# Performance work log

Hardware: AMD Instinct MI355X
Metric: run time of the kernel (lower is better)

## Reference

```python
import jax, jax.numpy as jnp
import numpy as np

N_NODES = 50000
N_GRAPHS = 1024


def _linear_params(key, fan_in, fan_out):
    k1, k2 = jax.random.split(key)
    lim = 1.0 / np.sqrt(fan_in)
    W = jax.random.uniform(k1, (fan_in, fan_out), minval=-lim, maxval=lim, dtype=jnp.float32)
    b = jax.random.uniform(k2, (fan_out,), minval=-lim, maxval=lim, dtype=jnp.float32)
    return W, b


def gcn_conv(x, W, b, src, dst, n):
    # PyG GCNConv: D^{-1/2} (A + I) D^{-1/2} X W + b, deg counted at target after self-loops
    h = x @ W                                   # [N, out]
    deg = jnp.zeros((n,), h.dtype).at[dst].add(1.0) + 1.0
    dinv = jax.lax.rsqrt(deg)
    norm = dinv[src] * dinv[dst]                # [E]
    msg = h[src] * norm[:, None]                # [E, out] (dominant traffic)
    agg = jax.ops.segment_sum(msg, dst, num_segments=n)
    agg = agg + h * (dinv * dinv)[:, None]      # self-loop contribution
    return agg + b


def setup_inputs() -> dict:
    key = jax.random.key(0)
    ks = jax.random.split(key, 16)
    x = jax.random.normal(ks[0], (N_NODES, 64), dtype=jnp.float32)
    edge_index = jax.random.randint(ks[1], (2, 800000), 0, N_NODES, dtype=jnp.int64)
    batch = jnp.sort(jax.random.randint(ks[2], (N_NODES,), 0, N_GRAPHS, dtype=jnp.int64))
    fingerprint_features = jax.random.uniform(ks[3], (N_GRAPHS, 2048), dtype=jnp.float32)
    func_groups = jax.random.uniform(ks[4], (N_GRAPHS, 167), dtype=jnp.float32)
    W1, b1 = _linear_params(ks[5], 64, 128)
    W2, b2 = _linear_params(ks[6], 128, 256)
    W3, b3 = _linear_params(ks[7], 256, 256)
    Wr1, br1 = _linear_params(ks[8], 128, 256)
    Wr2, br2 = _linear_params(ks[9], 256, 256)
    Wfp, bfp = _linear_params(ks[10], 2048, 256)
    Wfg, bfg = _linear_params(ks[11], 167, 256)
    attn_W = jax.random.uniform(ks[12], (256, 256), dtype=jnp.float32)
    Wfc, bfc = _linear_params(ks[13], 256, 1)
    return dict(x=x, edge_index=edge_index, batch=batch,
                fingerprint_features=fingerprint_features, func_groups=func_groups,
                W1=W1, b1=b1, W2=W2, b2=b2, W3=W3, b3=b3,
                Wr1=Wr1, br1=br1, Wr2=Wr2, br2=br2,
                Wfp=Wfp, bfp=bfp, Wfg=Wfg, bfg=bfg,
                attn_W=attn_W, Wfc=Wfc, bfc=bfc)


def reference(x, edge_index, batch, fingerprint_features, func_groups,
              W1, b1, W2, b2, W3, b3, Wr1, br1, Wr2, br2,
              Wfp, bfp, Wfg, bfg, attn_W, Wfc, bfc):
    n = x.shape[0]
    src, dst = edge_index[0], edge_index[1]
    x1 = jax.nn.relu(gcn_conv(x, W1, b1, src, dst, n))            # [N,128]
    # dropout inactive (eval mode)
    x2 = jax.nn.relu(gcn_conv(x1, W2, b2, src, dst, n) + x1 @ Wr1 + br1)  # [N,256]
    x3 = jax.nn.relu(gcn_conv(x2, W3, b3, src, dst, n) + x2 @ Wr2 + br2)  # [N,256]
    fp = jax.nn.relu(fingerprint_features @ Wfp + bfp)            # [B,256]
    fg = jax.nn.relu(func_groups @ Wfg + bfg)                     # [B,256]
    attn = jax.nn.softmax(x3 @ attn_W, axis=1)                    # [N,256]
    xw = attn * x3
    sums = jax.ops.segment_sum(xw, batch, num_segments=N_GRAPHS)  # [B,256]
    cnt = jax.ops.segment_sum(jnp.ones((n,), xw.dtype), batch, num_segments=N_GRAPHS)
    pooled = sums / jnp.maximum(cnt, 1.0)[:, None]                # global_mean_pool
    out = (pooled + fp + fg) @ Wfc + bfc                          # [B,1]
    return out.reshape(-1, 1)
```

## Files before the change

### kernel.cpp

```cpp
#include <hip/hip_runtime.h>
#include <math.h>

#define CDIV(a,b) (((a)+(b)-1)/(b))

typedef __attribute__((ext_vector_type(8))) short bf16x8;
typedef __attribute__((ext_vector_type(4))) float f32x4;

__device__ inline unsigned short f2bf(float f) {
    unsigned int u = __float_as_uint(f);
    u += 0x7fffu + ((u >> 16) & 1u);
    return (unsigned short)(u >> 16);
}
__device__ inline float bf2f(unsigned short h) { return __uint_as_float(((unsigned int)h) << 16); }
__device__ inline unsigned short f2h(float f) {
    _Float16 h = (_Float16)f;
    return *(unsigned short*)&h;
}
__device__ inline float h2f(unsigned short u) {
    _Float16 h = *(_Float16*)&u;
    return (float)h;
}

__global__ void deg_count_kernel(const int* __restrict__ dst, int* __restrict__ deg, int E) {
    int e = blockIdx.x * blockDim.x + threadIdx.x;
    if (e < E) atomicAdd(&deg[dst[e]], 1);
}

__global__ void dinv_kernel(const int* __restrict__ deg, float* __restrict__ dinv, int N) {
    int i = blockIdx.x * blockDim.x + threadIdx.x;
    if (i < N) dinv[i] = rsqrtf((float)deg[i] + 1.0f);
}

__global__ void chunk_sum_kernel(const int* __restrict__ deg, int* __restrict__ csum, int N) {
    __shared__ int ws[4];
    int c = blockIdx.x, t = threadIdx.x;
    int base = c * 1024;
    int s = 0;
    for (int i = t; i < 1024; i += 256) { int idx = base + i; s += (idx < N) ? deg[idx] : 0; }
    for (int o = 32; o; o >>= 1) s += __shfl_xor(s, o);
    if ((t & 63) == 0) ws[t >> 6] = s;
    __syncthreads();
    if (t == 0) csum[c] = ws[0] + ws[1] + ws[2] + ws[3];
}

__global__ void chunk_scan_kernel(int* __restrict__ csum, int nc) {
    int t = threadIdx.x;
    int v = (t < nc) ? csum[t] : 0;
    int x = v;
    #pragma unroll
    for (int o = 1; o < 64; o <<= 1) { int y = __shfl_up(x, o, 64); if (t >= o) x += y; }
    if (t < nc) csum[t] = x - v;
}

__global__ void chunk_scan_apply_kernel(const int* __restrict__ deg, const int* __restrict__ cbase,
                                        int* __restrict__ off, int N, int E) {
    __shared__ int wsum[16];
    int c = blockIdx.x;
    int t = threadIdx.x;
    int lane = t & 63, wid = t >> 6;
    int i = c * 1024 + t;
    int v = (i < N) ? deg[i] : 0;
    int x = v;
    #pragma unroll
    for (int o = 1; o < 64; o <<= 1) { int y = __shfl_up(x, o, 64); if (lane >= o) x += y; }
    if (lane == 63) wsum[wid] = x;
    __syncthreads();
    if (wid == 0) {
        int wv = (lane < 16) ? wsum[lane] : 0;
        #pragma unroll
        for (int o = 1; o < 16; o <<= 1) { int y = __shfl_up(wv, o, 64); if (lane >= o) wv += y; }
        if (lane < 16) wsum[lane] = wv;
    }
    __syncthreads();
    int wexcl = wid ? wsum[wid - 1] : 0;
    if (i < N) off[i] = cbase[c] + wexcl + x - v;
    if (i == N) off[N] = E;
}

__global__ void csr_fill_kernel(const int* __restrict__ src, const int* __restrict__ dst,
                                const int* __restrict__ off, int* __restrict__ pos,
                                int* __restrict__ csr_src, int E) {
    int e = blockIdx.x * blockDim.x + threadIdx.x;
    if (e >= E) return;
    int s = src[e], d = dst[e];
    int p = off[d] + atomicAdd(&pos[d], 1);
    csr_src[p] = s;
}

__global__ void split_kernel(const float* __restrict__ src, unsigned short* __restrict__ hi,
                             unsigned short* __restrict__ lo, long long total) {
    long long idx = (long long)blockIdx.x * blockDim.x + threadIdx.x;
    if (idx >= total) return;
    float v = src[idx];
    unsigned short h = f2bf(v);
    hi[idx] = h;
    lo[idx] = f2bf(v - bf2f(h));
}

__global__ void f32_to_f16_kernel(const float* __restrict__ src, unsigned short* __restrict__ dst,
                                  long long total) {
    long long idx = (long long)blockIdx.x * blockDim.x + threadIdx.x;
    if (idx >= total) return;
    dst[idx] = f2h(src[idx]);
}

__global__ void wsplit_t_kernel(const float* __restrict__ src, int K, int N,
                                unsigned short* __restrict__ dsth, unsigned short* __restrict__ dstl,
                                int ldt, int koff) {
    int idx = blockIdx.x * blockDim.x + threadIdx.x;
    if (idx >= K * N) return;
    int col = idx / K;
    int k = idx - col * K;
    float v = src[(size_t)k * N + col];
    unsigned short h = f2bf(v);
    size_t o = (size_t)col * ldt + koff + k;
    dsth[o] = h;
    dstl[o] = f2bf(v - bf2f(h));
}

__global__ void bsum_kernel(const float* __restrict__ a, const float* __restrict__ b,
                            float* __restrict__ dst, int n) {
    int j = blockIdx.x * blockDim.x + threadIdx.x;
    if (j < n) dst[j] = a[j] + b[j];
}

template<int F>
__global__ __launch_bounds__(F) void gcn_gather_kernel(
        const unsigned short* __restrict__ h16, int ldh,
        const float* __restrict__ dinv, const int* __restrict__ off,
        const int* __restrict__ csr_src,
        unsigned short* __restrict__ outh, unsigned short* __restrict__ outl,
        int ldo, int cofo) {
    const int n = blockIdx.x;
    const int j = threadIdx.x;
    float dd = dinv[n];
    float acc = h2f(h16[(size_t)n * ldh + j]) * dd * dd;
    const int e1 = off[n + 1];
    int e = off[n];
    for (; e + 4 <= e1; e += 4) {
        int s0 = csr_src[e], s1 = csr_src[e + 1], s2 = csr_src[e + 2], s3 = csr_src[e + 3];
        float n0 = dinv[s0] * dd, n1 = dinv[s1] * dd, n2 = dinv[s2] * dd, n3 = dinv[s3] * dd;
        float h0 = h2f(h16[(size_t)s0 * ldh + j]);
        float h1 = h2f(h16[(size_t)s1 * ldh + j]);
        float h2 = h2f(h16[(size_t)s2 * ldh + j]);
        float h3 = h2f(h16[(size_t)s3 * ldh + j]);
        acc += h0 * n0; acc += h1 * n1; acc += h2 * n2; acc += h3 * n3;
    }
    for (; e < e1; ++e) {
        int s0 = csr_src[e];
        acc += h2f(h16[(size_t)s0 * ldh + j]) * (dinv[s0] * dd);
    }
    size_t o = (size_t)n * ldo + cofo + j;
    unsigned short hv = f2bf(acc);
    outh[o] = hv;
    outl[o] = f2bf(acc - bf2f(hv));
}

__global__ __launch_bounds__(256) void mfma_gemm_kernel(
        const unsigned short* __restrict__ Ah, const unsigned short* __restrict__ Al, int lda,
        const unsigned short* __restrict__ Wth, const unsigned short* __restrict__ Wtl, int ldt,
        const float* __restrict__ bias,
        float* __restrict__ Cf32, int ldc,
        unsigned short* __restrict__ outh, unsigned short* __restrict__ outl, int ldo, int coff,
        unsigned short* __restrict__ outf16, int ldo16,
        int M, int K, int NW, int relu, int kchunk) {
    __shared__ unsigned short AsH[128 * 40];
    __shared__ unsigned short AsL[128 * 40];
    __shared__ unsigned short WsH[128 * 40];
    __shared__ unsigned short WsL[128 * 40];
    const int tid = threadIdx.x;
    const int row0 = blockIdx.x * 128;
    const int col0 = blockIdx.y * 128;
    int kbeg = 0, kend = K;
    size_t zoff = 0;
    if (kchunk) {
        kbeg = blockIdx.z * kchunk;
        kend = kbeg + kchunk;
        zoff = (size_t)blockIdx.z * M * NW;
    }
    const int w = tid >> 6, l = tid & 63;
    const int wm = w >> 1, wn = w & 1;
    const int lrow = l & 15, lk = l >> 4;
    f32x4 acc[4][4] = {};
    for (int k0 = kbeg; k0 < kend; k0 += 32) {
        #pragma unroll
        for (int i = 0; i < 2; ++i) {
            int c = tid * 2 + i;
            int r = c >> 2, kq = c & 3;
            int gr = row0 + r;
            uint4 vh = make_uint4(0, 0, 0, 0), vl = make_uint4(0, 0, 0, 0);
            if (gr < M) {
                size_t g = (size_t)gr * lda + k0 + kq * 8;
                vh = *(const uint4*)&Ah[g];
                vl = *(const uint4*)&Al[g];
            }
            *(uint4*)&AsH[r * 40 + kq * 8] = vh;
            *(uint4*)&AsL[r * 40 + kq * 8] = vl;
        }
        #pragma unroll
        for (int i = 0; i < 2; ++i) {
            int c = tid + i * 256;
            int col = c & 127, kq = c >> 7;
            size_t g = (size_t)(col0 + col) * ldt + k0 + kq * 8;
            uint4 vh = *(const uint4*)&Wth[g];
            uint4 vl = *(const uint4*)&Wtl[g];
            *(uint4*)&WsH[col * 40 + kq * 8] = vh;
            *(uint4*)&WsL[col * 40 + kq * 8] = vl;
        }
        __syncthreads();
        bf16x8 aH[4], aL[4], bH[4], bL[4];
        #pragma unroll
        for (int mi = 0; mi < 4; ++mi) {
            int r = wm * 64 + mi * 16 + lrow;
            aH[mi] = *(const bf16x8*)&AsH[r * 40 + lk * 8];
            aL[mi] = *(const bf16x8*)&AsL[r * 40 + lk * 8];
        }
        #pragma unroll
        for (int ni = 0; ni < 4; ++ni) {
            int cc = wn * 64 + ni * 16 + lrow;
            bH[ni] = *(const bf16x8*)&WsH[cc * 40 + lk * 8];
            bL[ni] = *(const bf16x8*)&WsL[cc * 40 + lk * 8];
        }
        #pragma unroll
        for (int mi = 0; mi < 4; ++mi)
            #pragma unroll
            for (int ni = 0; ni < 4; ++ni) {
                acc[mi][ni] = __builtin_amdgcn_mfma_f32_16x16x32_bf16(aH[mi], bH[ni], acc[mi][ni], 0, 0, 0);
                acc[mi][ni] = __builtin_amdgcn_mfma_f32_16x16x32_bf16(aH[mi], bL[ni], acc[mi][ni], 0, 0, 0);
                acc[mi][ni] = __builtin_amdgcn_mfma_f32_16x16x32_bf16(aL[mi], bH[ni], acc[mi][ni], 0, 0, 0);
            }
        __syncthreads();
    }
    #pragma unroll
    for (int mi = 0; mi < 4; ++mi) {
        #pragma unroll
        for (int ni = 0; ni < 4; ++ni) {
            int gc = col0 + wn * 64 + ni * 16 + lrow;
            float bb = bias ? bias[gc] : 0.f;
            #pragma unroll
            for (int q = 0; q < 4; ++q) {
                int gr = row0 + wm * 64 + mi * 16 + lk * 4 + q;
                if (gr >= M) continue;
                float v = acc[mi][ni][q] + bb;
                if (relu) v = fmaxf(v, 0.f);
                if (Cf32) Cf32[zoff + (size_t)gr * ldc + gc] = v;
                if (outh) {
                    size_t o = (size_t)gr * ldo + coff + gc;
                    unsigned short hv = f2bf(v);
                    outh[o] = hv;
                    outl[o] = f2bf(v - bf2f(hv));
                }
                if (outf16) outf16[(size_t)gr * ldo16 + gc] = f2h(v);
            }
        }
    }
}

__global__ void reduce_fp_kernel(const float* __restrict__ part, const float* __restrict__ bias,
                                 float* __restrict__ outp, int total, int stride, int nz) {
    int idx = blockIdx.x * blockDim.x + threadIdx.x;
    if (idx >= total) return;
    float s = 0.f;
    for (int z = 0; z < nz; ++z) s += part[(size_t)z * stride + idx];
    outp[idx] = fmaxf(s + bias[idx & 255], 0.f);
}

__global__ __launch_bounds__(256) void gemm_kernel(
        const float* __restrict__ A, const float* __restrict__ W,
        const float* __restrict__ bias, float* __restrict__ C,
        int M, int K, int N, int do_relu) {
    __shared__ float As[16][128];
    __shared__ float Ws[16][128];
    const int tid = threadIdx.x;
    const int tx = tid & 15;
    const int ty = tid >> 4;
    const int row0 = blockIdx.x * 128;
    const int col0 = blockIdx.y * 128;
    float acc[8][8] = {};
    for (int k0 = 0; k0 < K; k0 += 16) {
        #pragma unroll
        for (int i = 0; i < 2; ++i) {
            int s = tid * 2 + i;
            int r = s >> 2, c = (s & 3) << 2;
            int gr = row0 + r;
            float4 v = make_float4(0.f, 0.f, 0.f, 0.f);
            if (gr < M) {
                if (k0 + c + 3 < K) {
                    v = *(const float4*)(A + (size_t)gr * K + k0 + c);
                } else {
                    float t0 = (k0 + c     < K) ? A[(size_t)gr * K + k0 + c    ] : 0.f;
                    float t1 = (k0 + c + 1 < K) ? A[(size_t)gr * K + k0 + c + 1] : 0.f;
                    float t2 = (k0 + c + 2 < K) ? A[(size_t)gr * K + k0 + c + 2] : 0.f;
                    float t3 = (k0 + c + 3 < K) ? A[(size_t)gr * K + k0 + c + 3] : 0.f;
                    v = make_float4(t0, t1, t2, t3);
                }
            }
            As[c + 0][r] = v.x; As[c + 1][r] = v.y; As[c + 2][r] = v.z; As[c + 3][r] = v.w;
        }
        #pragma unroll
        for (int i = 0; i < 2; ++i) {
            int s = tid * 2 + i;
            int kk = s >> 5, c = (s & 31) << 2;
            int gk = k0 + kk, gc = col0 + c;
            float4 v = make_float4(0.f, 0.f, 0.f, 0.f);
            if (gk < K && gc + 3 < N) v = *(const float4*)(W + (size_t)gk * N + gc);
            *(float4*)&Ws[kk][c] = v;
        }
        __syncthreads();
        #pragma unroll
        for (int kk = 0; kk < 16; ++kk) {
            float a[8], b[8];
            *(float4*)&a[0] = *(const float4*)&As[kk][ty * 4];
            *(float4*)&a[4] = *(const float4*)&As[kk][ty * 4 + 64];
            *(float4*)&b[0] = *(const float4*)&Ws[kk][tx * 4];
            *(float4*)&b[4] = *(const float4*)&Ws[kk][tx * 4 + 64];
            #pragma unroll
            for (int i2 = 0; i2 < 8; ++i2)
                #pragma unroll
                for (int j2 = 0; j2 < 8; ++j2)
                    acc[i2][j2] += a[i2] * b[j2];
        }
        __syncthreads();
    }
    #pragma unroll
    for (int rh = 0; rh < 2; ++rh)
        #pragma unroll
        for (int ii = 0; ii < 4; ++ii) {
            int gr = row0 + ty * 4 + rh * 64 + ii;
            if (gr >= M) continue;
            #pragma unroll
            for (int ch = 0; ch < 2; ++ch) {
                int gc = col0 + tx * 4 + ch * 64;
                float v[4];
                #pragma unroll
                for (int q = 0; q < 4; ++q) {
                    v[q] = acc[rh * 4 + ii][ch * 4 + q] + (bias ? bias[gc + q] : 0.f);
                    if (do_relu) v[q] = fmaxf(v[q], 0.f);
                }
                if (gc + 3 < N)
                    *(float4*)(C + (size_t)gr * N + gc) = make_float4(v[0], v[1], v[2], v[3]);
            }
        }
}

__global__ __launch_bounds__(256) void softmaxpool_kernel(
        const float* __restrict__ logits, const unsigned short* __restrict__ x3f16,
        const int* __restrict__ batch, float* __restrict__ pooled, int N, int B) {
    __shared__ float lacc[4][256];
    const int b = blockIdx.x;
    const int t = threadIdx.x;
    const int lane = t & 63, wid = t >> 6;
    int lo = 0, hi = N;
    while (lo < hi) { int m = (lo + hi) >> 1; if (batch[m] < b) lo = m + 1; else hi = m; }
    int s0 = lo;
    hi = N;
    while (lo < hi) { int m = (lo + hi) >> 1; if (batch[m] <= b) lo = m + 1; else hi = m; }
    int s1 = lo;
    float a0 = 0.f, a1 = 0.f, a2 = 0.f, a3 = 0.f;
    for (int n = s0 + wid; n < s1; n += 4) {
        const float* p = logits + (size_t)n * 256;
        float v0 = p[lane], v1 = p[lane + 64], v2 = p[lane + 128], v3 = p[lane + 192];
        float m = fmaxf(fmaxf(v0, v1), fmaxf(v2, v3));
        for (int o = 32; o; o >>= 1) m = fmaxf(m, __shfl_xor(m, o));
        v0 = expf(v0 - m); v1 = expf(v1 - m); v2 = expf(v2 - m); v3 = expf(v3 - m);
        float s = v0 + v1 + v2 + v3;
        for (int o = 32; o; o >>= 1) s += __shfl_xor(s, o);
        float inv = 1.0f / s;
        const unsigned short* q = x3f16 + (size_t)n * 256;
        a0 += v0 * inv * h2f(q[lane]);
        a1 += v1 * inv * h2f(q[lane + 64]);
        a2 += v2 * inv * h2f(q[lane + 128]);
        a3 += v3 * inv * h2f(q[lane + 192]);
    }
    lacc[wid][lane] = a0; lacc[wid][lane + 64] = a1;
    lacc[wid][lane + 128] = a2; lacc[wid][lane + 192] = a3;
    __syncthreads();
    float tot = lacc[0][t] + lacc[1][t] + lacc[2][t] + lacc[3][t];
    float invc = 1.0f / fmaxf((float)(s1 - s0), 1.0f);
    pooled[(size_t)b * 256 + t] = tot * invc;
}

__global__ void final_kernel(const float* __restrict__ pooled, const float* __restrict__ fp,
                             const float* __restrict__ fg, const float* __restrict__ Wfc,
                             const float* __restrict__ bfc, float* __restrict__ out, int B) {
    int b = blockIdx.x * 4 + (threadIdx.x >> 6);
    int lane = threadIdx.x & 63;
    if (b >= B) return;
    float acc = 0.0f;
    #pragma unroll
    for (int i = 0; i < 4; ++i) {
        int j = lane + i * 64;
        size_t o = (size_t)b * 256 + j;
        acc += (pooled[o] + fp[o] + fg[o]) * Wfc[j];
    }
    for (int off = 32; off; off >>= 1) acc += __shfl_xor(acc, off);
    if (lane == 0) out[b] = acc + bfc[0];
}

extern "C" void kernel_launch(void* const* d_in, const int* in_sizes, int n_in,
                              void* d_out, int out_size, void* d_ws, size_t ws_size,
                              hipStream_t stream) {
    const float* x     = (const float*)d_in[0];
    const int*   ei    = (const int*)d_in[1];
    const int*   batch = (const int*)d_in[2];
    const float* fpin  = (const float*)d_in[3];
    const float* fgin  = (const float*)d_in[4];
    const float* W1  = (const float*)d_in[5];  const float* b1  = (const float*)d_in[6];
    const float* W2  = (const float*)d_in[7];  const float* b2  = (const float*)d_in[8];
    const float* W3  = (const float*)d_in[9];  const float* b3  = (const float*)d_in[10];
    const float* Wr1 = (const float*)d_in[11]; const float* br1 = (const float*)d_in[12];
    const float* Wr2 = (const float*)d_in[13]; const float* br2 = (const float*)d_in[14];
    const float* Wfp = (const float*)d_in[15]; const float* bfp = (const float*)d_in[16];
    const float* Wfg = (const float*)d_in[17]; const float* bfg = (const float*)d_in[18];
    const float* attnW = (const float*)d_in[19];
    const float* Wfc = (const float*)d_in[20]; const float* bfc = (const float*)d_in[21];
    float* out = (float*)d_out;

    const int Nn = in_sizes[0] / 64;
    const int E  = in_sizes[1] / 2;
    const int B  = in_sizes[3] / 2048;
    const int* src = ei;
    const int* dst = ei + E;

    char* wsb = (char*)d_ws;
    size_t woff = 0;
    auto alloc = [&](size_t bytes) -> void* {
        void* p = wsb + woff;
        woff += (bytes + 255) & ~(size_t)255;
        return p;
    };

    int*   deg_i   = (int*)alloc((size_t)Nn * 4);
    int*   pos     = (int*)alloc((size_t)Nn * 4);
    int*   offv    = (int*)alloc(((size_t)Nn + 1) * 4);
    float* dinv    = (float*)alloc((size_t)Nn * 4);
    int*   csum    = (int*)alloc(64 * 4);
    int*   csr_src = (int*)alloc((size_t)E * 4);
    unsigned short* W1th  = (unsigned short*)alloc(64 * 128 * 2);
    unsigned short* W1tl  = (unsigned short*)alloc(64 * 128 * 2);
    unsigned short* Wc2th = (unsigned short*)alloc(256 * 256 * 2);
    unsigned short* Wc2tl = (unsigned short*)alloc(256 * 256 * 2);
    unsigned short* Wc3th = (unsigned short*)alloc(512 * 256 * 2);
    unsigned short* Wc3tl = (unsigned short*)alloc(512 * 256 * 2);
    unsigned short* aWth  = (unsigned short*)alloc(256 * 256 * 2);
    unsigned short* aWtl  = (unsigned short*)alloc(256 * 256 * 2);
    unsigned short* Wfpth = (unsigned short*)alloc(2048 * 256 * 2);
    unsigned short* Wfptl = (unsigned short*)alloc(2048 * 256 * 2);
    float* bsum2 = (float*)alloc(256 * 4);
    float* bsum3 = (float*)alloc(256 * 4);
    unsigned short* Acat2h = (unsigned short*)alloc((size_t)Nn * 256 * 2);
    unsigned short* Acat2l = (unsigned short*)alloc((size_t)Nn * 256 * 2);
    unsigned short* Acat3h = (unsigned short*)alloc((size_t)Nn * 512 * 2);
    unsigned short* Acat3l = (unsigned short*)alloc((size_t)Nn * 512 * 2);
    unsigned short* x3h    = (unsigned short*)alloc((size_t)Nn * 256 * 2);
    unsigned short* x3l    = (unsigned short*)alloc((size_t)Nn * 256 * 2);
    unsigned short* x23f16 = (unsigned short*)alloc((size_t)Nn * 256 * 2);
    (void)ws_size; (void)n_in; (void)out_size;

    unsigned short* agg0h = Acat3h;
    unsigned short* xf16  = (unsigned short*)((char*)Acat3h + 8388608);
    unsigned short* agg0l = Acat3l;
    unsigned short* x1f16 = (unsigned short*)((char*)Acat3l + 8388608);
    float* logits = (float*)Acat3h;
    char* fpRegion = (char*)Acat3l;
    unsigned short* fpinh = (unsigned short*)(fpRegion);
    unsigned short* fpinl = (unsigned short*)(fpRegion + 4499968);
    float* part   = (float*)(fpRegion + 9000192);
    float* fpb    = (float*)(fpRegion + 17500160);
    float* fgb    = (float*)(fpRegion + 18600192);
    float* pooled = (float*)(fpRegion + 19700224);
    unsigned short* x2f16 = x23f16;
    unsigned short* x3f16 = x23f16;

    hipMemsetAsync(deg_i, 0, (size_t)Nn * 4, stream);
    hipMemsetAsync(pos,   0, (size_t)Nn * 4, stream);
    deg_count_kernel<<<CDIV(E, 256), 256, 0, stream>>>(dst, deg_i, E);
    dinv_kernel<<<CDIV(Nn, 256), 256, 0, stream>>>(deg_i, dinv, Nn);
    const int NC = CDIV(Nn, 1024);
    chunk_sum_kernel<<<NC, 256, 0, stream>>>(deg_i, csum, Nn);
    chunk_scan_kernel<<<1, 64, 0, stream>>>(csum, NC);
    chunk_scan_apply_kernel<<<NC, 1024, 0, stream>>>(deg_i, csum, offv, Nn, E);
    csr_fill_kernel<<<CDIV(E, 256), 256, 0, stream>>>(src, dst, offv, pos, csr_src, E);

    wsplit_t_kernel<<<CDIV(64 * 128, 256), 256, 0, stream>>>(W1, 64, 128, W1th, W1tl, 64, 0);
    wsplit_t_kernel<<<CDIV(128 * 256, 256), 256, 0, stream>>>(W2,  128, 256, Wc2th, Wc2tl, 256, 0);
    wsplit_t_kernel<<<CDIV(128 * 256, 256), 256, 0, stream>>>(Wr1, 128, 256, Wc2th, Wc2tl, 256, 128);
    wsplit_t_kernel<<<CDIV(256 * 256, 256), 256, 0, stream>>>(W3,  256, 256, Wc3th, Wc3tl, 512, 0);
    wsplit_t_kernel<<<CDIV(256 * 256, 256), 256, 0, stream>>>(Wr2, 256, 256, Wc3th, Wc3tl, 512, 256);
    wsplit_t_kernel<<<CDIV(256 * 256, 256), 256, 0, stream>>>(attnW, 256, 256, aWth, aWtl, 256, 0);
    wsplit_t_kernel<<<CDIV(2048 * 256, 256), 256, 0, stream>>>(Wfp, 2048, 256, Wfpth, Wfptl, 2048, 0);
    bsum_kernel<<<1, 256, 0, stream>>>(b2, br1, bsum2, 256);
    bsum_kernel<<<1, 256, 0, stream>>>(b3, br2, bsum3, 256);
    long long txin = (long long)Nn * 64;
    f32_to_f16_kernel<<<CDIV(txin, 256), 256, 0, stream>>>(x, xf16, txin);

    const int MB = CDIV(Nn, 128);

    gcn_gather_kernel<64><<<Nn, 64, 0, stream>>>(xf16, 64, dinv, offv, csr_src, agg0h, agg0l, 64, 0);
    mfma_gemm_kernel<<<dim3(MB, 1), 256, 0, stream>>>(agg0h, agg0l, 64, W1th, W1tl, 64,
                                                      b1, nullptr, 0, Acat2h, Acat2l, 256, 128,
                                                      x1f16, 128, Nn, 64, 128, 1, 0);

    gcn_gather_kernel<128><<<Nn, 128, 0, stream>>>(x1f16, 128, dinv, offv, csr_src,
                                                   Acat2h, Acat2l, 256, 0);
    mfma_gemm_kernel<<<dim3(MB, 2), 256, 0, stream>>>(Acat2h, Acat2l, 256, Wc2th, Wc2tl, 256,
                                                      bsum2, nullptr, 0, Acat3h, Acat3l, 512, 256,
                                                      x2f16, 256, Nn, 256, 256, 1, 0);

    gcn_gather_kernel<256><<<Nn, 256, 0, stream>>>(x2f16, 256, dinv, offv, csr_src,
                                                   Acat3h, Acat3l, 512, 0);
    mfma_gemm_kernel<<<dim3(MB, 2), 256, 0, stream>>>(Acat3h, Acat3l, 512, Wc3th, Wc3tl, 512,
                                                      bsum3, nullptr, 0, x3h, x3l, 256, 0,
                                                      x3f16, 256, Nn, 512, 256, 1, 0);

    mfma_gemm_kernel<<<dim3(MB, 2), 256, 0, stream>>>(x3h, x3l, 256, aWth, aWtl, 256,
                                                      nullptr, logits, 256, nullptr, nullptr, 0, 0,
                                                      nullptr, 0, Nn, 256, 256, 0, 0);

    long long tfp = (long long)B * 2048;
    split_kernel<<<CDIV(tfp, 256), 256, 0, stream>>>(fpin, fpinh, fpinl, tfp);
    mfma_gemm_kernel<<<dim3(CDIV(B, 128), 2, 8), 256, 0, stream>>>(fpinh, fpinl, 2048, Wfpth, Wfptl, 2048,
                                                                   nullptr, part, 256, nullptr, nullptr, 0, 0,
                                                                   nullptr, 0, B, 2048, 256, 0, 256);
    reduce_fp_kernel<<<CDIV(B * 256, 256), 256, 0, stream>>>(part, bfp, fpb, B * 256, B * 256, 8);

    gemm_kernel<<<dim3(CDIV(B, 128), 2), 256, 0, stream>>>(fgin, Wfg, bfg, fgb, B, 167, 256, 1);

    softmaxpool_kernel<<<B, 256, 0, stream>>>(logits, x3f16, batch, pooled, Nn, B);
    final_kernel<<<CDIV(B, 4), 256, 0, stream>>>(pooled, fpb, fgb, Wfc, bfc, out, B);
}
```

Before: 759.8 us.

## Store intermediate activations as single fp16 and split to bf16 hi/lo in GEMM

Activations between gather and GEMM stages are now kept as one fp16 array instead of separate bf16 hi/lo arrays. The GEMM converts fp16 to a bf16 hi/lo pair on the fly while loading tiles. The gather reads its fp16 input straight from the concatenated buffer written by the previous GEMM, which drops the duplicate x1/x2 fp16 copies and the split kernel. This roughly halves global traffic for activation writes and GEMM A-loads, but fp16 storage reduces precision and range of the intermediates.

```diff
diff --git a/kernel.cpp b/kernel.cpp
--- a/kernel.cpp
+++ b/kernel.cpp
@@ -87,16 +87,6 @@
     csr_src[p] = s;
 }
 
-__global__ void split_kernel(const float* __restrict__ src, unsigned short* __restrict__ hi,
-                             unsigned short* __restrict__ lo, long long total) {
-    long long idx = (long long)blockIdx.x * blockDim.x + threadIdx.x;
-    if (idx >= total) return;
-    float v = src[idx];
-    unsigned short h = f2bf(v);
-    hi[idx] = h;
-    lo[idx] = f2bf(v - bf2f(h));
-}
-
 __global__ void f32_to_f16_kernel(const float* __restrict__ src, unsigned short* __restrict__ dst,
                                   long long total) {
     long long idx = (long long)blockIdx.x * blockDim.x + threadIdx.x;
@@ -126,43 +116,38 @@
 
 template<int F>
 __global__ __launch_bounds__(F) void gcn_gather_kernel(
-        const unsigned short* __restrict__ h16, int ldh,
+        const unsigned short* __restrict__ h16, int ldh, int cofh,
         const float* __restrict__ dinv, const int* __restrict__ off,
         const int* __restrict__ csr_src,
-        unsigned short* __restrict__ outh, unsigned short* __restrict__ outl,
-        int ldo, int cofo) {
+        unsigned short* __restrict__ out16, int ldo, int cofo) {
     const int n = blockIdx.x;
     const int j = threadIdx.x;
     float dd = dinv[n];
-    float acc = h2f(h16[(size_t)n * ldh + j]) * dd * dd;
+    float acc = h2f(h16[(size_t)n * ldh + cofh + j]) * dd * dd;
     const int e1 = off[n + 1];
     int e = off[n];
     for (; e + 4 <= e1; e += 4) {
         int s0 = csr_src[e], s1 = csr_src[e + 1], s2 = csr_src[e + 2], s3 = csr_src[e + 3];
         float n0 = dinv[s0] * dd, n1 = dinv[s1] * dd, n2 = dinv[s2] * dd, n3 = dinv[s3] * dd;
-        float h0 = h2f(h16[(size_t)s0 * ldh + j]);
-        float h1 = h2f(h16[(size_t)s1 * ldh + j]);
-        float h2 = h2f(h16[(size_t)s2 * ldh + j]);
-        float h3 = h2f(h16[(size_t)s3 * ldh + j]);
+        float h0 = h2f(h16[(size_t)s0 * ldh + cofh + j]);
+        float h1 = h2f(h16[(size_t)s1 * ldh + cofh + j]);
+        float h2 = h2f(h16[(size_t)s2 * ldh + cofh + j]);
+        float h3 = h2f(h16[(size_t)s3 * ldh + cofh + j]);
         acc += h0 * n0; acc += h1 * n1; acc += h2 * n2; acc += h3 * n3;
     }
     for (; e < e1; ++e) {
         int s0 = csr_src[e];
-        acc += h2f(h16[(size_t)s0 * ldh + j]) * (dinv[s0] * dd);
-    }
-    size_t o = (size_t)n * ldo + cofo + j;
-    unsigned short hv = f2bf(acc);
-    outh[o] = hv;
-    outl[o] = f2bf(acc - bf2f(hv));
+        acc += h2f(h16[(size_t)s0 * ldh + cofh + j]) * (dinv[s0] * dd);
+    }
+    out16[(size_t)n * ldo + cofo + j] = f2h(acc);
 }
 
 __global__ __launch_bounds__(256) void mfma_gemm_kernel(
-        const unsigned short* __restrict__ Ah, const unsigned short* __restrict__ Al, int lda,
+        const unsigned short* __restrict__ Af16, int lda,
         const unsigned short* __restrict__ Wth, const unsigned short* __restrict__ Wtl, int ldt,
         const float* __restrict__ bias,
         float* __restrict__ Cf32, int ldc,
-        unsigned short* __restrict__ outh, unsigned short* __restrict__ outl, int ldo, int coff,
-        unsigned short* __restrict__ outf16, int ldo16,
+        unsigned short* __restrict__ outf16, int ldo16, int cof16,
         int M, int K, int NW, int relu, int kchunk) {
     __shared__ unsigned short AsH[128 * 40];
     __shared__ unsigned short AsL[128 * 40];
@@ -188,14 +173,20 @@
             int c = tid * 2 + i;
             int r = c >> 2, kq = c & 3;
             int gr = row0 + r;
-            uint4 vh = make_uint4(0, 0, 0, 0), vl = make_uint4(0, 0, 0, 0);
-            if (gr < M) {
-                size_t g = (size_t)gr * lda + k0 + kq * 8;
-                vh = *(const uint4*)&Ah[g];
-                vl = *(const uint4*)&Al[g];
+            uint4 va = make_uint4(0, 0, 0, 0);
+            if (gr < M) va = *(const uint4*)&Af16[(size_t)gr * lda + k0 + kq * 8];
+            union { unsigned short us[8]; uint4 v; } hb, lb;
+            const unsigned short* pu = (const unsigned short*)&va;
+            #pragma unroll
+            for (int q = 0; q < 8; ++q) {
+                float f = h2f(pu[q]);
+                unsigned int uf = __float_as_uint(f);
+                hb.us[q] = (unsigned short)(uf >> 16);
+                float r2 = f - __uint_as_float(uf & 0xFFFF0000u);
+                lb.us[q] = (unsigned short)(__float_as_uint(r2) >> 16);
             }
-            *(uint4*)&AsH[r * 40 + kq * 8] = vh;
-            *(uint4*)&AsL[r * 40 + kq * 8] = vl;
+            *(uint4*)&AsH[r * 40 + kq * 8] = hb.v;
+            *(uint4*)&AsL[r * 40 + kq * 8] = lb.v;
         }
         #pragma unroll
         for (int i = 0; i < 2; ++i) {
@@ -244,13 +235,7 @@
                 float v = acc[mi][ni][q] + bb;
                 if (relu) v = fmaxf(v, 0.f);
                 if (Cf32) Cf32[zoff + (size_t)gr * ldc + gc] = v;
-                if (outh) {
-                    size_t o = (size_t)gr * ldo + coff + gc;
-                    unsigned short hv = f2bf(v);
-                    outh[o] = hv;
-                    outl[o] = f2bf(v - bf2f(hv));
-                }
-                if (outf16) outf16[(size_t)gr * ldo16 + gc] = f2h(v);
+                if (outf16) outf16[(size_t)gr * ldo16 + cof16 + gc] = f2h(v);
             }
         }
     }
@@ -448,29 +433,20 @@
     unsigned short* Wfptl = (unsigned short*)alloc(2048 * 256 * 2);
     float* bsum2 = (float*)alloc(256 * 4);
     float* bsum3 = (float*)alloc(256 * 4);
-    unsigned short* Acat2h = (unsigned short*)alloc((size_t)Nn * 256 * 2);
-    unsigned short* Acat2l = (unsigned short*)alloc((size_t)Nn * 256 * 2);
-    unsigned short* Acat3h = (unsigned short*)alloc((size_t)Nn * 512 * 2);
-    unsigned short* Acat3l = (unsigned short*)alloc((size_t)Nn * 512 * 2);
-    unsigned short* x3h    = (unsigned short*)alloc((size_t)Nn * 256 * 2);
-    unsigned short* x3l    = (unsigned short*)alloc((size_t)Nn * 256 * 2);
-    unsigned short* x23f16 = (unsigned short*)alloc((size_t)Nn * 256 * 2);
+    unsigned short* Acat2f16 = (unsigned short*)alloc((size_t)Nn * 256 * 2);
+    unsigned short* Acat3f16 = (unsigned short*)alloc((size_t)Nn * 512 * 2);
+    unsigned short* x3f16    = (unsigned short*)alloc((size_t)Nn * 256 * 2);
     (void)ws_size; (void)n_in; (void)out_size;
 
-    unsigned short* agg0h = Acat3h;
-    unsigned short* xf16  = (unsigned short*)((char*)Acat3h + 8388608);
-    unsigned short* agg0l = Acat3l;
-    unsigned short* x1f16 = (unsigned short*)((char*)Acat3l + 8388608);
-    float* logits = (float*)Acat3h;
-    char* fpRegion = (char*)Acat3l;
-    unsigned short* fpinh = (unsigned short*)(fpRegion);
-    unsigned short* fpinl = (unsigned short*)(fpRegion + 4499968);
-    float* part   = (float*)(fpRegion + 9000192);
-    float* fpb    = (float*)(fpRegion + 17500160);
-    float* fgb    = (float*)(fpRegion + 18600192);
-    float* pooled = (float*)(fpRegion + 19700224);
-    unsigned short* x2f16 = x23f16;
-    unsigned short* x3f16 = x23f16;
+    unsigned short* agg0f16 = Acat3f16;
+    unsigned short* xf16    = (unsigned short*)((char*)Acat3f16 + 8388608);
+    float* logits = (float*)Acat3f16;
+    char* fpRegion = (char*)Acat2f16;
+    unsigned short* fpin16 = (unsigned short*)(fpRegion);
+    float* part   = (float*)(fpRegion + 4718592);
+    float* fpb    = (float*)(fpRegion + 13631488);
+    float* fgb    = (float*)(fpRegion + 14680064);
+    float* pooled = (float*)(fpRegion + 15728640);
 
     hipMemsetAsync(deg_i, 0, (size_t)Nn * 4, stream);
     hipMemsetAsync(pos,   0, (size_t)Nn * 4, stream);
@@ -496,32 +472,32 @@
 
     const int MB = CDIV(Nn, 128);
 
-    gcn_gather_kernel<64><<<Nn, 64, 0, stream>>>(xf16, 64, dinv, offv, csr_src, agg0h, agg0l, 64, 0);
-    mfma_gemm_kernel<<<dim3(MB, 1), 256, 0, stream>>>(agg0h, agg0l, 64, W1th, W1tl, 64,
-                                                      b1, nullptr, 0, Acat2h, Acat2l, 256, 128,
-                                                      x1f16, 128, Nn, 64, 128, 1, 0);
-
-    gcn_gather_kernel<128><<<Nn, 128, 0, stream>>>(x1f16, 128, dinv, offv, csr_src,
-                                                   Acat2h, Acat2l, 256, 0);
-    mfma_gemm_kernel<<<dim3(MB, 2), 256, 0, stream>>>(Acat2h, Acat2l, 256, Wc2th, Wc2tl, 256,
-                                                      bsum2, nullptr, 0, Acat3h, Acat3l, 512, 256,
-                                                      x2f16, 256, Nn, 256, 256, 1, 0);
-
-    gcn_gather_kernel<256><<<Nn, 256, 0, stream>>>(x2f16, 256, dinv, offv, csr_src,
-                                                   Acat3h, Acat3l, 512, 0);
-    mfma_gemm_kernel<<<dim3(MB, 2), 256, 0, stream>>>(Acat3h, Acat3l, 512, Wc3th, Wc3tl, 512,
-                                                      bsum3, nullptr, 0, x3h, x3l, 256, 0,
-                                                      x3f16, 256, Nn, 512, 256, 1, 0);
-
-    mfma_gemm_kernel<<<dim3(MB, 2), 256, 0, stream>>>(x3h, x3l, 256, aWth, aWtl, 256,
-                                                      nullptr, logits, 256, nullptr, nullptr, 0, 0,
-                                                      nullptr, 0, Nn, 256, 256, 0, 0);
+    gcn_gather_kernel<64><<<Nn, 64, 0, stream>>>(xf16, 64, 0, dinv, offv, csr_src, agg0f16, 64, 0);
+    mfma_gemm_kernel<<<dim3(MB, 1), 256, 0, stream>>>(agg0f16, 64, W1th, W1tl, 64,
+                                                      b1, nullptr, 0, Acat2f16, 256, 128,
+                                                      Nn, 64, 128, 1, 0);
+
+    gcn_gather_kernel<128><<<Nn, 128, 0, stream>>>(Acat2f16, 256, 128, dinv, offv, csr_src,
+                                                   Acat2f16, 256, 0);
+    mfma_gemm_kernel<<<dim3(MB, 2), 256, 0, stream>>>(Acat2f16, 256, Wc2th, Wc2tl, 256,
+                                                      bsum2, nullptr, 0, Acat3f16, 512, 256,
+                                                      Nn, 256, 256, 1, 0);
+
+    gcn_gather_kernel<256><<<Nn, 256, 0, stream>>>(Acat3f16, 512, 256, dinv, offv, csr_src,
+                                                   Acat3f16, 512, 0);
+    mfma_gemm_kernel<<<dim3(MB, 2), 256, 0, stream>>>(Acat3f16, 512, Wc3th, Wc3tl, 512,
+                                                      bsum3, nullptr, 0, x3f16, 256, 0,
+                                                      Nn, 512, 256, 1, 0);
+
+    mfma_gemm_kernel<<<dim3(MB, 2), 256, 0, stream>>>(x3f16, 256, aWth, aWtl, 256,
+                                                      nullptr, logits, 256, nullptr, 0, 0,
+                                                      Nn, 256, 256, 0, 0);
 
     long long tfp = (long long)B * 2048;
-    split_kernel<<<CDIV(tfp, 256), 256, 0, stream>>>(fpin, fpinh, fpinl, tfp);
-    mfma_gemm_kernel<<<dim3(CDIV(B, 128), 2, 8), 256, 0, stream>>>(fpinh, fpinl, 2048, Wfpth, Wfptl, 2048,
-                                                                   nullptr, part, 256, nullptr, nullptr, 0, 0,
-                                                                   nullptr, 0, B, 2048, 256, 0, 256);
+    f32_to_f16_kernel<<<CDIV(tfp, 256), 256, 0, stream>>>(fpin, fpin16, tfp);
+    mfma_gemm_kernel<<<dim3(CDIV(B, 128), 2, 8), 256, 0, stream>>>(fpin16, 2048, Wfpth, Wfptl, 2048,
+                                                                   nullptr, part, 256, nullptr, 0, 0,
+                                                                   B, 2048, 256, 0, 256);
     reduce_fp_kernel<<<CDIV(B * 256, 256), 256, 0, stream>>>(part, bfp, fpb, B * 256, B * 256, 8);
 
     gemm_kernel<<<dim3(CDIV(B, 128), 2), 256, 0, stream>>>(fgin, Wfg, bfg, fgb, B, 167, 256, 1);
```

After: 698.0 us. 8.1% less time.
